# Performance work log

Hardware: AMD Instinct MI355X
Metric: run time of the kernel (lower is better)

## Reference

```python
import jax, jax.numpy as jnp
import numpy as np

HID = 1024
HEADS = 16
DH = HID // HEADS
SCALE = DH ** -0.5
L, B = 2048, 2


def setup_inputs() -> dict:
    key = jax.random.key(0)
    ks = jax.random.split(key, 16)
    inp = {
        "query": jax.random.normal(ks[0], (L, B, HID), jnp.float32),
        "key": jax.random.normal(ks[1], (L, B, HID), jnp.float32),
        "value": jax.random.normal(ks[2], (L, B, HID), jnp.float32),
        "mask": jax.random.randint(ks[3], (B, L), 0, 2).astype(bool),
    }
    # xavier-uniform linear weights (torch Linear stores [out, in]; y = x @ W.T + b)
    lim = (6.0 / (HID + HID)) ** 0.5
    for i, name in enumerate(["wq", "wk", "wv", "wfc"]):
        inp[name] = jax.random.uniform(ks[4 + i], (HID, HID), jnp.float32, -lim, lim)
    inp["bq"] = jnp.zeros((HID,), jnp.float32)
    inp["bk"] = jnp.zeros((HID,), jnp.float32)
    inp["bv"] = jnp.zeros((HID,), jnp.float32)
    inp["bfc"] = jnp.zeros((HID,), jnp.float32)
    inp["tao"] = jnp.full((HEADS,), 10.0, jnp.float32)
    return inp


def reference(query, key, value, mask, wq, bq, wk, bk, wv, bv, wfc, bfc, tao):
    # inputs arrive [L, B, D]; module transposes to [B, L, D]
    q = jnp.swapaxes(query, 0, 1)
    k = jnp.swapaxes(key, 0, 1)
    v = jnp.swapaxes(value, 0, 1)
    bsz, length, _ = q.shape

    def heads(x, w, b):
        y = x @ w.T + b                      # [B, L, D]
        return y.reshape(bsz, length, HEADS, DH).transpose(0, 2, 1, 3)  # [B, H, L, d]

    Q = heads(q, wq, bq)
    K = heads(k, wk, bk)
    V = heads(v, wv, bv)

    qk = jnp.einsum("bhqd,bhkd->bhqk", Q, K) * SCALE  # [B, H, L, L]

    # gaussian positional bias: -|i-j|^2/2 * tao_h^-4
    idx = jnp.arange(length, dtype=jnp.float32)
    dist = -0.5 * (idx[:, None] - idx[None, :]) ** 2          # [L, L]
    qk = qk + dist[None, None, :, :] * (tao ** -4)[None, :, None, None]

    qk = jnp.where(mask[:, None, None, :], -jnp.inf, qk)
    attn = jax.nn.softmax(qk, axis=-1)  # dropout is identity in eval mode

    x = jnp.einsum("bhqk,bhkd->bhqd", attn, V)            # [B, H, L, d]
    x = x.transpose(0, 2, 1, 3).reshape(bsz, length, HID)  # [B, L, D]
    x = x @ wfc.T + bfc
    return jnp.swapaxes(x, 0, 1)  # [L, B, D]
```

## Files before the change

### kernel.cpp

```cpp
#include <hip/hip_runtime.h>

#define LQ   2048
#define BQ   2
#define HID  1024
#define NH   16
#define DH   64
#define SCALE 0.125f
#define L2E  1.44269504088896f
#define C1   0.18033688011f
#define EXPOFF 23.0831206542f
#define MASKNEG (-1024.0f)

using short8  = __attribute__((ext_vector_type(8))) short;
using ushort8 = __attribute__((ext_vector_type(8))) unsigned short;
using f32x4   = __attribute__((ext_vector_type(4))) float;
typedef unsigned short u16;
typedef __attribute__((ext_vector_type(2))) __bf16 bf16x2;

__device__ inline u16 f2bf(float x) {
    unsigned int u = __float_as_uint(x);
    u = (u + 0x7fffu + ((u >> 16) & 1u)) >> 16;
    return (u16)u;
}

#if defined(__has_builtin)
#if __has_builtin(__builtin_amdgcn_cvt_pk_bf16_f32)
#define HAVE_PKBF 1
#endif
#if __has_builtin(__builtin_amdgcn_exp2f)
#define HAVE_EXP2 1
#endif
#endif

__device__ inline unsigned int pkbf(float a, float b) {
#ifdef HAVE_PKBF
    bf16x2 r = __builtin_amdgcn_cvt_pk_bf16_f32(a, b);
    return __builtin_bit_cast(unsigned int, r);
#else
    return (unsigned int)f2bf(a) | ((unsigned int)f2bf(b) << 16);
#endif
}

__device__ inline float fexp2(float x) {
#ifdef HAVE_EXP2
    return __builtin_amdgcn_exp2f(x);
#else
    return exp2f(x);
#endif
}

__device__ inline void gl_lds16(const void* g, void* l) {
    __builtin_amdgcn_global_load_lds(
        (const __attribute__((address_space(1))) void*)g,
        (__attribute__((address_space(3))) void*)l, 16, 0, 0);
}

struct CastArgs {
    const float* s[7];
    u16* d[7];
    int n[7];
    const unsigned char* mraw;
    float* mout;
    int mn;
};

__global__ __launch_bounds__(256) void castw(CastArgs a) {
    const int y = blockIdx.y;
    const int t = threadIdx.x;
    if (y == 7) {
        if (blockIdx.x != 0) return;
        __shared__ int cnt;
        if (t == 0) cnt = 0;
        __syncthreads();
        int local = 0;
        for (int i = t; i < a.mn; i += 256)
            if ((i & 3) && a.mraw[i]) local++;
        atomicAdd(&cnt, local);
        __syncthreads();
        bool isInt32 = (cnt == 0);
        const int* mi = (const int*)a.mraw;
        for (int i = t; i < a.mn; i += 256) {
            const bool m = isInt32 ? (mi[i] != 0) : (a.mraw[i] != 0);
            a.mout[i] = m ? (MASKNEG - EXPOFF) : (-EXPOFF);
        }
        return;
    }
    const float* s = a.s[y];
    u16* d = a.d[y];
    const int n4 = a.n[y] >> 2;
    for (int i = blockIdx.x * 256 + t; i < n4; i += gridDim.x * 256) {
        float4 v = *(const float4*)(s + (size_t)i * 4);
        uint2 p;
        p.x = pkbf(v.x, v.y);
        p.y = pkbf(v.z, v.w);
        *(uint2*)(d + (size_t)i * 4) = p;
    }
}

struct QkvArgs {
    const u16* A[3];
    const u16* W[3];
    const float* bias[3];
    u16* out[3];
};

__global__ __launch_bounds__(256) void gemm_qkv(QkvArgs ga) {
    __shared__ u16 As[2][128][64];
    __shared__ u16 Bs[2][128][64];

    const int z = blockIdx.z;
    const u16* A = ga.A[z];
    const u16* W = ga.W[z];
    const float* bias = ga.bias[z];
    u16* outp = ga.out[z];

    const int t = threadIdx.x;
    const int m0 = blockIdx.x * 128;
    const int n0 = blockIdx.y * 128;
    const int lane = t & 63;
    const int lane15 = lane & 15;
    const int quad = lane >> 4;
    const int w = t >> 6;
    const int wm = (w >> 1) * 64;
    const int wn = (w & 1) * 64;

    const int lrow = lane >> 3;
    const int ch = (lane & 7) ^ ((lane >> 3) & 7);
    const u16* aS = A + (size_t)(m0 + 32 * w + lrow) * HID + 8 * ch;
    const u16* bS = W + (size_t)(n0 + 32 * w + lrow) * HID + 8 * ch;

    const int s0 = (quad ^ (lane15 & 7)) * 8;
    const int s1 = ((4 + quad) ^ (lane15 & 7)) * 8;

    f32x4 acc[4][4];
#pragma unroll
    for (int i = 0; i < 4; i++)
#pragma unroll
        for (int j = 0; j < 4; j++) acc[i][j] = (f32x4){0,0,0,0};

#pragma unroll
    for (int i = 0; i < 4; i++) {
        gl_lds16(aS + (size_t)(8 * i) * HID, &As[0][32 * w + 8 * i][0]);
        gl_lds16(bS + (size_t)(8 * i) * HID, &Bs[0][32 * w + 8 * i][0]);
    }
    __syncthreads();

    int p = 0;
    for (int k0 = 0; k0 < HID; k0 += 64) {
        short8 af0[4], af1[4], bf0[4], bf1[4];
#pragma unroll
        for (int i = 0; i < 4; i++) {
            const u16* ar = &As[p][wm + i * 16 + lane15][0];
            const u16* br = &Bs[p][wn + i * 16 + lane15][0];
            af0[i] = *(const short8*)(ar + s0);
            af1[i] = *(const short8*)(ar + s1);
            bf0[i] = *(const short8*)(br + s0);
            bf1[i] = *(const short8*)(br + s1);
        }
        if (k0 + 64 < HID) {
#pragma unroll
            for (int i = 0; i < 4; i++) {
                gl_lds16(aS + (size_t)(8 * i) * HID + (k0 + 64), &As[p ^ 1][32 * w + 8 * i][0]);
                gl_lds16(bS + (size_t)(8 * i) * HID + (k0 + 64), &Bs[p ^ 1][32 * w + 8 * i][0]);
            }
        }
#pragma unroll
        for (int mi = 0; mi < 4; mi++)
#pragma unroll
            for (int ni = 0; ni < 4; ni++) {
                acc[mi][ni] = __builtin_amdgcn_mfma_f32_16x16x32_bf16(af0[mi], bf0[ni], acc[mi][ni], 0, 0, 0);
                acc[mi][ni] = __builtin_amdgcn_mfma_f32_16x16x32_bf16(af1[mi], bf1[ni], acc[mi][ni], 0, 0, 0);
            }
        __syncthreads();
        p ^= 1;
    }

#pragma unroll
    for (int mi = 0; mi < 4; mi++) {
#pragma unroll
        for (int ni = 0; ni < 4; ni++) {
            const int n = n0 + wn + ni * 16 + lane15;
            const float bv = bias[n];
            const int h = n >> 6, d = n & 63;
#pragma unroll
            for (int r = 0; r < 4; r++) {
                const int m = m0 + wm + mi * 16 + quad * 4 + r;
                const float c = acc[mi][ni][r] + bv;
                const int b = m & 1, l = m >> 1;
                if (z < 2) {
                    outp[(((size_t)(b * NH + h)) * LQ + l) * DH + d] = f2bf(c);
                } else {
                    outp[(((size_t)(b * NH + h)) * DH + d) * LQ + l] = f2bf(c);
                }
            }
        }
    }
}

__global__ __launch_bounds__(256) void gemm_fc(const u16* __restrict__ A,
                                               const u16* __restrict__ W,
                                               const float* __restrict__ bias,
                                               float* __restrict__ outp) {
    __shared__ u16 As[2][128][64];
    __shared__ u16 Bs[2][64][64];

    const int t = threadIdx.x;
    const int m0 = blockIdx.x * 128;
    const int n0 = blockIdx.y * 64;
    const int lane = t & 63;
    const int lane15 = lane & 15;
    const int quad = lane >> 4;
    const int w = t >> 6;
    const int wm = (w >> 1) * 64;
    const int wn = (w & 1) * 32;

    const int lrow = lane >> 3;
    const int ch = (lane & 7) ^ ((lane >> 3) & 7);
    const u16* aS = A + (size_t)(m0 + 32 * w + lrow) * HID + 8 * ch;
    const u16* bS = W + (size_t)(n0 + 16 * w + lrow) * HID + 8 * ch;

    const int s0 = (quad ^ (lane15 & 7)) * 8;
    const int s1 = ((4 + quad) ^ (lane15 & 7)) * 8;

    f32x4 acc[4][2];
#pragma unroll
    for (int i = 0; i < 4; i++)
#pragma unroll
        for (int j = 0; j < 2; j++) acc[i][j] = (f32x4){0,0,0,0};

#pragma unroll
    for (int i = 0; i < 4; i++)
        gl_lds16(aS + (size_t)(8 * i) * HID, &As[0][32 * w + 8 * i][0]);
#pragma unroll
    for (int i = 0; i < 2; i++)
        gl_lds16(bS + (size_t)(8 * i) * HID, &Bs[0][16 * w + 8 * i][0]);
    __syncthreads();

    int p = 0;
    for (int k0 = 0; k0 < HID; k0 += 64) {
        short8 af0[4], af1[4], bf0[2], bf1[2];
#pragma unroll
        for (int i = 0; i < 4; i++) {
            const u16* ar = &As[p][wm + i * 16 + lane15][0];
            af0[i] = *(const short8*)(ar + s0);
            af1[i] = *(const short8*)(ar + s1);
        }
#pragma unroll
        for (int j = 0; j < 2; j++) {
            const u16* br = &Bs[p][wn + j * 16 + lane15][0];
            bf0[j] = *(const short8*)(br + s0);
            bf1[j] = *(const short8*)(br + s1);
        }
        if (k0 + 64 < HID) {
#pragma unroll
            for (int i = 0; i < 4; i++)
                gl_lds16(aS + (size_t)(8 * i) * HID + (k0 + 64), &As[p ^ 1][32 * w + 8 * i][0]);
#pragma unroll
            for (int i = 0; i < 2; i++)
                gl_lds16(bS + (size_t)(8 * i) * HID + (k0 + 64), &Bs[p ^ 1][16 * w + 8 * i][0]);
        }
#pragma unroll
        for (int mi = 0; mi < 4; mi++)
#pragma unroll
            for (int ni = 0; ni < 2; ni++) {
                acc[mi][ni] = __builtin_amdgcn_mfma_f32_16x16x32_bf16(af0[mi], bf0[ni], acc[mi][ni], 0, 0, 0);
                acc[mi][ni] = __builtin_amdgcn_mfma_f32_16x16x32_bf16(af1[mi], bf1[ni], acc[mi][ni], 0, 0, 0);
            }
        __syncthreads();
        p ^= 1;
    }

#pragma unroll
    for (int mi = 0; mi < 4; mi++) {
#pragma unroll
        for (int ni = 0; ni < 2; ni++) {
            const int n = n0 + wn + ni * 16 + lane15;
            const float bv = bias[n];
#pragma unroll
            for (int r = 0; r < 4; r++) {
                const int m = m0 + wm + mi * 16 + quad * 4 + r;
                outp[(size_t)m * HID + n] = acc[mi][ni][r] + bv;
            }
        }
    }
}

#define PSTR 72

__global__ __launch_bounds__(256, 2) void attn_kernel(const u16* __restrict__ Qg,
                                                      const u16* __restrict__ Kg,
                                                      const u16* __restrict__ Vtg,
                                                      const float* __restrict__ maskF,
                                                      const float* __restrict__ tao,
                                                      u16* __restrict__ Xa) {
    __shared__ u16 Ks[2][64][64];
    __shared__ u16 Vt[2][64][64];
    __shared__ u16 PT[128][PSTR];

    const int bh = blockIdx.x;
    const int q0 = blockIdx.y * 128;
    const int b = bh >> 4;
    const int h = bh & 15;
    const int t = threadIdx.x;
    const int w = t >> 6;
    const int lane = t & 63;
    const int lane15 = lane & 15;
    const int quad = lane >> 4;

    const u16* Kbase = Kg + (size_t)bh * LQ * DH;
    const u16* Vtbase = Vtg + (size_t)bh * DH * LQ;
    const float* mrow = maskF + b * LQ;

    const float tv = tao[h];
    const float t2 = tv * tv;
    const float nb = -0.5f / (t2 * t2);
    const float nb2 = nb * L2E;
    const float sqn = sqrtf(-nb2);
    const float R = sqrtf(-40.0f / nb2) + 1.0f;

    int c_lo = (int)floorf(((float)q0 - R) * (1.0f / 64.0f));
    int c_hi = (int)floorf(((float)(q0 + 127) + R) * (1.0f / 64.0f));
    if (c_lo < 0) c_lo = 0;
    if (c_hi > (LQ / 64 - 1)) c_hi = LQ / 64 - 1;
    if (c_hi < c_lo) c_hi = c_lo;

    const int lr = lane >> 3;
    const int sch = (lane & 7) ^ lr;
    const u16* kS0 = Kbase + (size_t)(16 * w + lr) * DH + 8 * sch;
    const u16* kS1 = Kbase + (size_t)(16 * w + 8 + lr) * DH + 8 * sch;
    const u16* vS0 = Vtbase + (size_t)(16 * w + lr) * LQ + 8 * sch;
    const u16* vS1 = Vtbase + (size_t)(16 * w + 8 + lr) * LQ + 8 * sch;

    const int qrow0 = q0 + w * 32 + lane15;
    const int qrow1 = qrow0 + 16;
    short8 qA00, qA01, qA10, qA11;
    {
        const u16* qp0 = Qg + ((size_t)bh * LQ + qrow0) * DH + quad * 8;
        qA00 = *(const short8*)(qp0);
        qA01 = *(const short8*)(qp0 + 32);
        const u16* qp1 = Qg + ((size_t)bh * LQ + qrow1) * DH + quad * 8;
        qA10 = *(const short8*)(qp1);
        qA11 = *(const short8*)(qp1 + 32);
    }

    const int s0 = (quad ^ (lane15 & 7)) * 8;
    const int s1 = ((4 + quad) ^ (lane15 & 7)) * 8;

    float crs[16];
#pragma unroll
    for (int i = 0; i < 16; i++)
        crs[i] = (float)((i >> 2) * 16 + (i & 3)) * sqn;

    short8 ones;
#pragma unroll
    for (int i = 0; i < 8; i++) ones[i] = (short)0x3F80;

    f32x4 O0[4], O1[4];
#pragma unroll
    for (int mt = 0; mt < 4; mt++) { O0[mt] = (f32x4){0,0,0,0}; O1[mt] = (f32x4){0,0,0,0}; }
    f32x4 Lac0 = (f32x4){0,0,0,0};
    f32x4 Lac1 = (f32x4){0,0,0,0};

    const float eb00 = (float)(qrow0 - quad * 4);
    const float eb01 = (float)(qrow1 - quad * 4);
    const int prow0 = w * 32 + lane15;
    const int prow1 = prow0 + 16;

    gl_lds16(kS0 + (size_t)c_lo * (64 * DH), &Ks[0][16 * w][0]);
    gl_lds16(kS1 + (size_t)c_lo * (64 * DH), &Ks[0][16 * w + 8][0]);
    gl_lds16(vS0 + 64 * c_lo, &Vt[0][16 * w][0]);
    gl_lds16(vS1 + 64 * c_lo, &Vt[0][16 * w + 8][0]);
    __syncthreads();

    int p = 0;
    for (int c = c_lo; c <= c_hi; ++c) {
        float4 mv[4];
#pragma unroll
        for (int kt = 0; kt < 4; kt++)
            mv[kt] = *(const float4*)(mrow + 64 * c + kt * 16 + quad * 4);

        if (c < c_hi) {
            gl_lds16(kS0 + (size_t)(c + 1) * (64 * DH), &Ks[p ^ 1][16 * w][0]);
            gl_lds16(kS1 + (size_t)(c + 1) * (64 * DH), &Ks[p ^ 1][16 * w + 8][0]);
            gl_lds16(vS0 + 64 * (c + 1), &Vt[p ^ 1][16 * w][0]);
            gl_lds16(vS1 + 64 * (c + 1), &Vt[p ^ 1][16 * w + 8][0]);
        }

        f32x4 S0[4], S1[4];
#pragma unroll
        for (int kt = 0; kt < 4; kt++) {
            const u16* kr = &Ks[p][kt * 16 + lane15][0];
            const short8 ka = *(const short8*)(kr + s0);
            const short8 kb = *(const short8*)(kr + s1);
            S0[kt] = __builtin_amdgcn_mfma_f32_16x16x32_bf16(ka, qA00, (f32x4){0,0,0,0}, 0, 0, 0);
            S0[kt] = __builtin_amdgcn_mfma_f32_16x16x32_bf16(kb, qA01, S0[kt], 0, 0, 0);
            S1[kt] = __builtin_amdgcn_mfma_f32_16x16x32_bf16(ka, qA10, (f32x4){0,0,0,0}, 0, 0, 0);
            S1[kt] = __builtin_amdgcn_mfma_f32_16x16x32_bf16(kb, qA11, S1[kt], 0, 0, 0);
        }

        const float ebS0 = (eb00 - (float)(64 * c)) * sqn;
        const float ebS1 = (eb01 - (float)(64 * c)) * sqn;
#pragma unroll
        for (int kt = 0; kt < 4; kt++) {
            float pr0[4], pr1[4];
#pragma unroll
            for (int r = 0; r < 4; r++) {
                const float mb = ((const float*)&mv[kt])[r];
                const float dp0 = ebS0 - crs[kt * 4 + r];
                const float dp1 = ebS1 - crs[kt * 4 + r];
                pr0[r] = fexp2(fmaf(S0[kt][r], C1, fmaf(-dp0, dp0, mb)));
                pr1[r] = fexp2(fmaf(S1[kt][r], C1, fmaf(-dp1, dp1, mb)));
            }
            uint2 pk0, pk1;
            pk0.x = pkbf(pr0[0], pr0[1]);
            pk0.y = pkbf(pr0[2], pr0[3]);
            pk1.x = pkbf(pr1[0], pr1[1]);
            pk1.y = pkbf(pr1[2], pr1[3]);
            *(uint2*)&PT[prow0][kt * 16 + quad * 4] = pk0;
            *(uint2*)&PT[prow1][kt * 16 + quad * 4] = pk1;
        }

        const short8 pB00 = *(const short8*)&PT[prow0][quad * 8];
        const short8 pB01 = *(const short8*)&PT[prow0][32 + quad * 8];
        const short8 pB10 = *(const short8*)&PT[prow1][quad * 8];
        const short8 pB11 = *(const short8*)&PT[prow1][32 + quad * 8];
        Lac0 = __builtin_amdgcn_mfma_f32_16x16x32_bf16(ones, pB00, Lac0, 0, 0, 0);
        Lac0 = __builtin_amdgcn_mfma_f32_16x16x32_bf16(ones, pB01, Lac0, 0, 0, 0);
        Lac1 = __builtin_amdgcn_mfma_f32_16x16x32_bf16(ones, pB10, Lac1, 0, 0, 0);
        Lac1 = __builtin_amdgcn_mfma_f32_16x16x32_bf16(ones, pB11, Lac1, 0, 0, 0);

#pragma unroll
        for (int mt = 0; mt < 4; mt++) {
            const u16* vr = &Vt[p][mt * 16 + lane15][0];
            const short8 va = *(const short8*)(vr + s0);
            const short8 vb = *(const short8*)(vr + s1);
            O0[mt] = __builtin_amdgcn_mfma_f32_16x16x32_bf16(va, pB00, O0[mt], 0, 0, 0);
            O0[mt] = __builtin_amdgcn_mfma_f32_16x16x32_bf16(vb, pB01, O0[mt], 0, 0, 0);
            O1[mt] = __builtin_amdgcn_mfma_f32_16x16x32_bf16(va, pB10, O1[mt], 0, 0, 0);
            O1[mt] = __builtin_amdgcn_mfma_f32_16x16x32_bf16(vb, pB11, O1[mt], 0, 0, 0);
        }

        __syncthreads();
        p ^= 1;
    }

    {
        const float inv0 = 1.0f / Lac0[0];
        u16* dst0 = Xa + ((size_t)qrow0 * BQ + b) * HID + h * DH;
#pragma unroll
        for (int mt = 0; mt < 4; mt++) {
            uint2 pk2;
            pk2.x = pkbf(O0[mt][0] * inv0, O0[mt][1] * inv0);
            pk2.y = pkbf(O0[mt][2] * inv0, O0[mt][3] * inv0);
            *(uint2*)(dst0 + mt * 16 + quad * 4) = pk2;
        }
        const float inv1 = 1.0f / Lac1[0];
        u16* dst1 = Xa + ((size_t)qrow1 * BQ + b) * HID + h * DH;
#pragma unroll
        for (int mt = 0; mt < 4; mt++) {
            uint2 pk2;
            pk2.x = pkbf(O1[mt][0] * inv1, O1[mt][1] * inv1);
            pk2.y = pkbf(O1[mt][2] * inv1, O1[mt][3] * inv1);
            *(uint2*)(dst1 + mt * 16 + quad * 4) = pk2;
        }
    }
}

extern "C" void kernel_launch(void* const* d_in, const int* in_sizes, int n_in,
                              void* d_out, int out_size, void* d_ws, size_t ws_size,
                              hipStream_t stream) {
    const float* q    = (const float*)d_in[0];
    const float* k    = (const float*)d_in[1];
    const float* v    = (const float*)d_in[2];
    const void*  mask = d_in[3];
    const float* wq   = (const float*)d_in[4];
    const float* wk   = (const float*)d_in[5];
    const float* wv   = (const float*)d_in[6];
    const float* wfc  = (const float*)d_in[7];
    const float* bq   = (const float*)d_in[8];
    const float* bk   = (const float*)d_in[9];
    const float* bv   = (const float*)d_in[10];
    const float* bfc  = (const float*)d_in[11];
    const float* tao  = (const float*)d_in[12];

    const size_t NE = (size_t)LQ * BQ * HID;
    const size_t NW = (size_t)HID * HID;
    u16* base = (u16*)d_ws;
    u16* Qp    = base;
    u16* Kp    = base + NE;
    u16* Vtp   = base + 2 * NE;
    u16* Xa    = base + 3 * NE;
    u16* qbf   = base + 4 * NE;
    u16* kbf   = base + 5 * NE;
    u16* vbf   = base + 6 * NE;
    u16* wqbf  = base + 7 * NE;
    u16* wkbf  = wqbf + NW;
    u16* wvbf  = wkbf + NW;
    u16* wfcbf = wvbf + NW;
    float* maskF = (float*)(wfcbf + NW);

    CastArgs ca;
    ca.s[0] = q;   ca.d[0] = qbf;   ca.n[0] = (int)NE;
    ca.s[1] = k;   ca.d[1] = kbf;   ca.n[1] = (int)NE;
    ca.s[2] = v;   ca.d[2] = vbf;   ca.n[2] = (int)NE;
    ca.s[3] = wq;  ca.d[3] = wqbf;  ca.n[3] = (int)NW;
    ca.s[4] = wk;  ca.d[4] = wkbf;  ca.n[4] = (int)NW;
    ca.s[5] = wv;  ca.d[5] = wvbf;  ca.n[5] = (int)NW;
    ca.s[6] = wfc; ca.d[6] = wfcbf; ca.n[6] = (int)NW;
    ca.mraw = (const unsigned char*)mask;
    ca.mout = maskF;
    ca.mn = BQ * LQ;
    castw<<<dim3(256, 8), 256, 0, stream>>>(ca);

    QkvArgs ga;
    ga.A[0] = qbf;  ga.W[0] = wqbf;  ga.bias[0] = bq;  ga.out[0] = Qp;
    ga.A[1] = kbf;  ga.W[1] = wkbf;  ga.bias[1] = bk;  ga.out[1] = Kp;
    ga.A[2] = vbf;  ga.W[2] = wvbf;  ga.bias[2] = bv;  ga.out[2] = Vtp;
    gemm_qkv<<<dim3(32, 8, 3), 256, 0, stream>>>(ga);

    attn_kernel<<<dim3(32, 16), 256, 0, stream>>>(Qp, Kp, Vtp, maskF, tao, Xa);

    gemm_fc<<<dim3(32, 16), 256, 0, stream>>>(Xa, wfcbf, bfc, (float*)d_out);
}
```

Before: 231.5 us.

## Prefetch two K-tiles ahead in projection GEMMs with explicit vmcnt waits

Both the QKV projection and output FC GEMMs now keep two K-tiles of global-to-LDS loads in flight instead of one. Explicit s_waitcnt vmcnt counts and split barriers replace the single __syncthreads per iteration. The next-next tile is issued into the just-consumed buffer after the fragments are read into registers. The goal is to hide global load latency behind MFMA work, at the cost of hand-managed wait counts that must match the number of loads issued per stage.

```diff
diff --git a/kernel.cpp b/kernel.cpp
--- a/kernel.cpp
+++ b/kernel.cpp
@@ -53,6 +53,16 @@
     __builtin_amdgcn_global_load_lds(
         (const __attribute__((address_space(1))) void*)g,
         (__attribute__((address_space(3))) void*)l, 16, 0, 0);
+}
+
+__device__ inline void wvm8() { asm volatile("s_waitcnt vmcnt(8)" ::: "memory"); __builtin_amdgcn_sched_barrier(0); }
+__device__ inline void wvm6() { asm volatile("s_waitcnt vmcnt(6)" ::: "memory"); __builtin_amdgcn_sched_barrier(0); }
+__device__ inline void wvm0() { asm volatile("s_waitcnt vmcnt(0)" ::: "memory"); __builtin_amdgcn_sched_barrier(0); }
+__device__ inline void wlg0() { asm volatile("s_waitcnt lgkmcnt(0)" ::: "memory"); __builtin_amdgcn_sched_barrier(0); }
+__device__ inline void sbar() {
+    __builtin_amdgcn_sched_barrier(0);
+    __builtin_amdgcn_s_barrier();
+    __builtin_amdgcn_sched_barrier(0);
 }
 
 struct CastArgs {
@@ -138,32 +148,37 @@
 #pragma unroll
         for (int j = 0; j < 4; j++) acc[i][j] = (f32x4){0,0,0,0};
 
-#pragma unroll
-    for (int i = 0; i < 4; i++) {
-        gl_lds16(aS + (size_t)(8 * i) * HID, &As[0][32 * w + 8 * i][0]);
-        gl_lds16(bS + (size_t)(8 * i) * HID, &Bs[0][32 * w + 8 * i][0]);
-    }
-    __syncthreads();
-
-    int p = 0;
-    for (int k0 = 0; k0 < HID; k0 += 64) {
+#define QKV_STAGE(kt, buf)                                                          \
+    {                                                                               \
+        _Pragma("unroll")                                                           \
+        for (int i = 0; i < 4; i++) {                                               \
+            gl_lds16(aS + (size_t)(8 * i) * HID + 64 * (kt), &As[buf][32 * w + 8 * i][0]); \
+            gl_lds16(bS + (size_t)(8 * i) * HID + 64 * (kt), &Bs[buf][32 * w + 8 * i][0]); \
+        }                                                                           \
+    }
+
+    QKV_STAGE(0, 0);
+    QKV_STAGE(1, 1);
+
+    for (int kt = 0; kt < 16; ++kt) {
+        if (kt < 15) wvm8(); else wvm0();
+        sbar();
+
+        const int pb = kt & 1;
         short8 af0[4], af1[4], bf0[4], bf1[4];
 #pragma unroll
         for (int i = 0; i < 4; i++) {
-            const u16* ar = &As[p][wm + i * 16 + lane15][0];
-            const u16* br = &Bs[p][wn + i * 16 + lane15][0];
+            const u16* ar = &As[pb][wm + i * 16 + lane15][0];
+            const u16* br = &Bs[pb][wn + i * 16 + lane15][0];
             af0[i] = *(const short8*)(ar + s0);
             af1[i] = *(const short8*)(ar + s1);
             bf0[i] = *(const short8*)(br + s0);
             bf1[i] = *(const short8*)(br + s1);
         }
-        if (k0 + 64 < HID) {
-#pragma unroll
-            for (int i = 0; i < 4; i++) {
-                gl_lds16(aS + (size_t)(8 * i) * HID + (k0 + 64), &As[p ^ 1][32 * w + 8 * i][0]);
-                gl_lds16(bS + (size_t)(8 * i) * HID + (k0 + 64), &Bs[p ^ 1][32 * w + 8 * i][0]);
-            }
-        }
+        wlg0();
+        sbar();
+        if (kt + 2 < 16) QKV_STAGE(kt + 2, pb);
+
 #pragma unroll
         for (int mi = 0; mi < 4; mi++)
 #pragma unroll
@@ -171,9 +186,8 @@
                 acc[mi][ni] = __builtin_amdgcn_mfma_f32_16x16x32_bf16(af0[mi], bf0[ni], acc[mi][ni], 0, 0, 0);
                 acc[mi][ni] = __builtin_amdgcn_mfma_f32_16x16x32_bf16(af1[mi], bf1[ni], acc[mi][ni], 0, 0, 0);
             }
-        __syncthreads();
-        p ^= 1;
-    }
+    }
+#undef QKV_STAGE
 
 #pragma unroll
     for (int mi = 0; mi < 4; mi++) {
@@ -228,37 +242,41 @@
 #pragma unroll
         for (int j = 0; j < 2; j++) acc[i][j] = (f32x4){0,0,0,0};
 
-#pragma unroll
-    for (int i = 0; i < 4; i++)
-        gl_lds16(aS + (size_t)(8 * i) * HID, &As[0][32 * w + 8 * i][0]);
-#pragma unroll
-    for (int i = 0; i < 2; i++)
-        gl_lds16(bS + (size_t)(8 * i) * HID, &Bs[0][16 * w + 8 * i][0]);
-    __syncthreads();
-
-    int p = 0;
-    for (int k0 = 0; k0 < HID; k0 += 64) {
+#define FC_STAGE(kt, buf)                                                           \
+    {                                                                               \
+        _Pragma("unroll")                                                           \
+        for (int i = 0; i < 4; i++)                                                 \
+            gl_lds16(aS + (size_t)(8 * i) * HID + 64 * (kt), &As[buf][32 * w + 8 * i][0]); \
+        _Pragma("unroll")                                                           \
+        for (int i = 0; i < 2; i++)                                                 \
+            gl_lds16(bS + (size_t)(8 * i) * HID + 64 * (kt), &Bs[buf][16 * w + 8 * i][0]); \
+    }
+
+    FC_STAGE(0, 0);
+    FC_STAGE(1, 1);
+
+    for (int kt = 0; kt < 16; ++kt) {
+        if (kt < 15) wvm6(); else wvm0();
+        sbar();
+
+        const int pb = kt & 1;
         short8 af0[4], af1[4], bf0[2], bf1[2];
 #pragma unroll
         for (int i = 0; i < 4; i++) {
-            const u16* ar = &As[p][wm + i * 16 + lane15][0];
+            const u16* ar = &As[pb][wm + i * 16 + lane15][0];
             af0[i] = *(const short8*)(ar + s0);
             af1[i] = *(const short8*)(ar + s1);
         }
 #pragma unroll
         for (int j = 0; j < 2; j++) {
-            const u16* br = &Bs[p][wn + j * 16 + lane15][0];
+            const u16* br = &Bs[pb][wn + j * 16 + lane15][0];
             bf0[j] = *(const short8*)(br + s0);
             bf1[j] = *(const short8*)(br + s1);
         }
-        if (k0 + 64 < HID) {
-#pragma unroll
-            for (int i = 0; i < 4; i++)
-                gl_lds16(aS + (size_t)(8 * i) * HID + (k0 + 64), &As[p ^ 1][32 * w + 8 * i][0]);
-#pragma unroll
-            for (int i = 0; i < 2; i++)
-                gl_lds16(bS + (size_t)(8 * i) * HID + (k0 + 64), &Bs[p ^ 1][16 * w + 8 * i][0]);
-        }
+        wlg0();
+        sbar();
+        if (kt + 2 < 16) FC_STAGE(kt + 2, pb);
+
 #pragma unroll
         for (int mi = 0; mi < 4; mi++)
 #pragma unroll
@@ -266,9 +284,8 @@
                 acc[mi][ni] = __builtin_amdgcn_mfma_f32_16x16x32_bf16(af0[mi], bf0[ni], acc[mi][ni], 0, 0, 0);
                 acc[mi][ni] = __builtin_amdgcn_mfma_f32_16x16x32_bf16(af1[mi], bf1[ni], acc[mi][ni], 0, 0, 0);
             }
-        __syncthreads();
-        p ^= 1;
-    }
+    }
+#undef FC_STAGE
 
 #pragma unroll
     for (int mi = 0; mi < 4; mi++) {
```

New measurement: 237.5 us. 2.6% more time.
